# Optimization experiments

Hardware: AMD Instinct MI355X
Metric: run time of the kernel (lower is better)

The kernel has to match this reference:

```python
import jax, jax.numpy as jnp
import numpy as np

VOCAB = 32000
WDIM = 768      # bert-base hidden size, per self.w_dim
H = 512         # lstm_hidden
NUM_CAT = 5
START = 3       # l2ind['SOS']
END = 4         # l2ind['EOS']
T = 2048
NEG = -10000.0


def _lstm_dir(x, Wih, Whh, bih, bhh, reverse):
    # x: [T, WDIM]; torch LSTM gate order: i, f, g, o
    z_in = x @ Wih.T + bih + bhh  # [T, 4H] precompute input projection
    def step(carry, zt):
        h, c = carry
        z = zt + h @ Whh.T
        i, f, g, o = jnp.split(z, 4)
        c = jax.nn.sigmoid(f) * c + jax.nn.sigmoid(i) * jnp.tanh(g)
        h = jax.nn.sigmoid(o) * jnp.tanh(c)
        return (h, c), h
    init = (jnp.zeros((H,), x.dtype), jnp.zeros((H,), x.dtype))
    _, hs = jax.lax.scan(step, init, z_in, reverse=reverse)
    return hs  # [T, H], aligned with input order


def setup_inputs():
    key = jax.random.key(0)
    ks = jax.random.split(key, 13)
    s = 0.05
    sent = jax.random.randint(ks[0], (T,), 0, VOCAB)
    emb = jax.random.normal(ks[1], (VOCAB, WDIM), jnp.float32) * 0.02
    Wih_f = jax.random.normal(ks[2], (4 * H, WDIM), jnp.float32) * s
    Whh_f = jax.random.normal(ks[3], (4 * H, H), jnp.float32) * s
    bih_f = jax.random.normal(ks[4], (4 * H,), jnp.float32) * s
    bhh_f = jax.random.normal(ks[5], (4 * H,), jnp.float32) * s
    Wih_b = jax.random.normal(ks[6], (4 * H, WDIM), jnp.float32) * s
    Whh_b = jax.random.normal(ks[7], (4 * H, H), jnp.float32) * s
    bih_b = jax.random.normal(ks[8], (4 * H,), jnp.float32) * s
    bhh_b = jax.random.normal(ks[9], (4 * H,), jnp.float32) * s
    fc_w = jax.random.normal(ks[10], (NUM_CAT, 2 * H), jnp.float32) * s
    fc_b = jax.random.normal(ks[11], (NUM_CAT,), jnp.float32) * s
    transitions = jax.random.normal(ks[12], (NUM_CAT, NUM_CAT), jnp.float32)
    transitions = transitions.at[START, :].set(NEG).at[:, END].set(NEG)
    return {"sent": sent, "emb": emb,
            "Wih_f": Wih_f, "Whh_f": Whh_f, "bih_f": bih_f, "bhh_f": bhh_f,
            "Wih_b": Wih_b, "Whh_b": Whh_b, "bih_b": bih_b, "bhh_b": bhh_b,
            "fc_w": fc_w, "fc_b": fc_b, "transitions": transitions}


def reference(sent, emb, Wih_f, Whh_f, bih_f, bhh_f, Wih_b, Whh_b, bih_b, bhh_b, fc_w, fc_b, transitions):
    # _get_scores: embedding -> BiLSTM -> fc
    x = emb[sent]                                   # [T, WDIM]
    h_f = _lstm_dir(x, Wih_f, Whh_f, bih_f, bhh_f, reverse=False)
    h_b = _lstm_dir(x, Wih_b, Whh_b, bih_b, bhh_b, reverse=True)
    out = jnp.concatenate([h_f, h_b], axis=-1)      # [T, 2H]
    feats = out @ fc_w.T + fc_b                     # [T, NUM_CAT]

    # _viterbi_decode: transitions[i, j] = score of moving from tag j to tag i
    init = feats[0] + transitions[:, START]         # [NUM_CAT]
    def vstep(layer, feat_t):
        # scores[i, j] = feat_t[i] + transitions[i, j] + layer[j]
        scores = feat_t[:, None] + transitions + layer[None, :]
        return jnp.max(scores, axis=1), jnp.argmax(scores, axis=1)
    layer, parents = jax.lax.scan(vstep, init, feats[1:])  # parents: [T-1, NUM_CAT]

    final = layer + transitions[END]
    idx0 = jnp.argmax(final)
    path_score = jnp.max(final)

    # backtrack (parents[0] of the original loop is all-START and gets popped)
    def btrack(idx, p):
        nxt = p[idx]
        return nxt, nxt
    _, idxs = jax.lax.scan(btrack, idx0, parents, reverse=True)  # [T-1]
    path = jnp.concatenate([idxs, idx0[None]])      # [T]
    return path, path_score
```

## Files before the change

kernel.cpp:

```cpp
#include <hip/hip_runtime.h>

#define TT 2048
#define WD 768
#define HH 512
#define G4 2048
#define NC 5
#define SENT 0xFFFFFFFFu

typedef float f4 __attribute__((ext_vector_type(4)));
typedef unsigned int u4 __attribute__((ext_vector_type(4)));

__global__ __launch_bounds__(256) void zin_gemm(
    const int* __restrict__ sent, const float* __restrict__ emb,
    const float* __restrict__ Wih_f, const float* __restrict__ bih_f, const float* __restrict__ bhh_f,
    const float* __restrict__ Wih_b, const float* __restrict__ bih_b, const float* __restrict__ bhh_b,
    float* __restrict__ zin_f, float* __restrict__ zin_b)
{
    const int dirn = blockIdx.z;
    const float* Wih = dirn ? Wih_b : Wih_f;
    const float* bih = dirn ? bih_b : bih_f;
    const float* bhh = dirn ? bhh_b : bhh_f;
    float* zin = dirn ? zin_b : zin_f;

    __shared__ float As[16][128];
    __shared__ float Bs[16][128];

    const int tid = threadIdx.x;
    const int t0 = blockIdx.y * 128;
    const int g0 = blockIdx.x * 128;
    const int tm = tid >> 4, tn = tid & 15;

    float acc[8][8];
#pragma unroll
    for (int a = 0; a < 8; a++)
#pragma unroll
        for (int b = 0; b < 8; b++) acc[a][b] = 0.f;

    for (int kt = 0; kt < 48; ++kt) {
        const int k0 = kt * 16;
#pragma unroll
        for (int u = 0; u < 2; ++u) {
            const int s = tid * 2 + u;
            const int m = s >> 2, kq = s & 3;
            const int rowA = sent[t0 + m];
            float4 av = *(const float4*)(emb + (size_t)rowA * WD + k0 + kq * 4);
            As[kq * 4 + 0][m] = av.x; As[kq * 4 + 1][m] = av.y;
            As[kq * 4 + 2][m] = av.z; As[kq * 4 + 3][m] = av.w;
            float4 bv = *(const float4*)(Wih + (size_t)(g0 + m) * WD + k0 + kq * 4);
            Bs[kq * 4 + 0][m] = bv.x; Bs[kq * 4 + 1][m] = bv.y;
            Bs[kq * 4 + 2][m] = bv.z; Bs[kq * 4 + 3][m] = bv.w;
        }
        __syncthreads();
#pragma unroll
        for (int kk = 0; kk < 16; ++kk) {
            float4 a0 = *(const float4*)&As[kk][tm * 8];
            float4 a1 = *(const float4*)&As[kk][tm * 8 + 4];
            float4 b0 = *(const float4*)&Bs[kk][tn * 8];
            float4 b1 = *(const float4*)&Bs[kk][tn * 8 + 4];
            float av8[8] = {a0.x, a0.y, a0.z, a0.w, a1.x, a1.y, a1.z, a1.w};
            float bv8[8] = {b0.x, b0.y, b0.z, b0.w, b1.x, b1.y, b1.z, b1.w};
#pragma unroll
            for (int a = 0; a < 8; a++)
#pragma unroll
                for (int b = 0; b < 8; b++) acc[a][b] += av8[a] * bv8[b];
        }
        __syncthreads();
    }
    float bias[8];
#pragma unroll
    for (int b = 0; b < 8; b++) { int g = g0 + tn * 8 + b; bias[b] = bih[g] + bhh[g]; }
#pragma unroll
    for (int a = 0; a < 8; a++) {
        const int t = t0 + tm * 8 + a;
        float* op = zin + (size_t)t * G4 + g0 + tn * 8;
        float4 o0 = {acc[a][0] + bias[0], acc[a][1] + bias[1], acc[a][2] + bias[2], acc[a][3] + bias[3]};
        float4 o1 = {acc[a][4] + bias[4], acc[a][5] + bias[5], acc[a][6] + bias[6], acc[a][7] + bias[7]};
        *(float4*)op = o0; *(float4*)(op + 4) = o1;
    }
}

__global__ __launch_bounds__(256, 1) void lstm_rec(
    const float* __restrict__ zin_f, const float* __restrict__ zin_b,
    const float* __restrict__ Whh_f, const float* __restrict__ Whh_b,
    unsigned int* __restrict__ hw_f, unsigned int* __restrict__ hw_b)
{
    const int bid = blockIdx.x;
    const int d = bid >> 5;
    const int k = bid & 31;
    const float* zin = d ? zin_b : zin_f;
    const float* Whh = d ? Whh_b : Whh_f;
    unsigned int* hw = d ? hw_b : hw_f;

    const int tid = threadIdx.x;
    const int q = tid >> 6;
    const int r = tid & 63;
    const int gate = r >> 4, jj = r & 15;
    const int grow = gate * HH + k * 16 + jj;

    const f4* wp = (const f4*)(Whh + (size_t)grow * HH + q * 128);
    f4 w[32];
#pragma unroll
    for (int i = 0; i < 32; ++i) w[i] = wp[i];
#pragma unroll
    for (int i = 0; i < 32; ++i)
        asm volatile("" : "+a"(w[i]));

    __shared__ float hs[HH];
    __shared__ float zb[256];

    float c = 0.f;
    const int l = tid;
    const int g = l >> 4, j = l & 15;
    const int n16 = k * 16 + j;

    for (int it = 0; it < TT; ++it) {
        const int t = d ? (TT - 1 - it) : it;

        float z = 0.f;
        if (tid < 64) z = zin[(size_t)t * G4 + g * HH + n16];

        if (it > 0 && tid < 64) {
            const int tp = d ? (t + 1) : (t - 1);
            const unsigned int* pa = hw + (size_t)tp * HH + l * 8;
            u4 a0, a1;
            for (;;) {
                asm volatile(
                    "global_load_dwordx4 %0, %2, off sc0 sc1\n\t"
                    "global_load_dwordx4 %1, %2, off offset:16 sc0 sc1\n\t"
                    "s_waitcnt vmcnt(0)"
                    : "=v"(a0), "=v"(a1) : "v"(pa) : "memory");
                if (a0.x != SENT && a0.y != SENT && a0.z != SENT && a0.w != SENT &&
                    a1.x != SENT && a1.y != SENT && a1.z != SENT && a1.w != SENT) break;
            }
            u4* hd = (u4*)(hs + l * 8);
            hd[0] = a0; hd[1] = a1;
        }
        __syncthreads();

#pragma unroll
        for (int i = 0; i < 32; ++i) asm volatile("" : "+a"(w[i]));

        float part = 0.f;
        if (it > 0) {
            const f4* hv = ((const f4*)hs) + (q << 5);
#pragma unroll
            for (int i = 0; i < 32; ++i) {
                f4 h4 = hv[i];
                part += w[i].x * h4.x + w[i].y * h4.y + w[i].z * h4.z + w[i].w * h4.w;
            }
        }
        zb[tid] = part;
        __syncthreads();

        if (tid < 64) {
            float s = zb[l] + zb[64 + l] + zb[128 + l] + zb[192 + l];
            const float pre = z + s;
            float act;
            if (g == 2) act = tanhf(pre);
            else        act = 1.f / (1.f + expf(-pre));
            const float gi = __shfl(act, j);
            const float gf = __shfl(act, j + 16);
            const float gg = __shfl(act, j + 32);
            const float go = __shfl(act, j + 48);
            if (l < 16) {
                c = gf * c + gi * gg;
                const float hval = go * tanhf(c);
                __hip_atomic_store(&hw[(size_t)t * HH + k * 16 + l],
                                   __float_as_uint(hval),
                                   __ATOMIC_RELAXED, __HIP_MEMORY_SCOPE_AGENT);
            }
        }
    }
}

__global__ void feats_kernel(const float* __restrict__ h_f, const float* __restrict__ h_b,
                             const float* __restrict__ fc_w, const float* __restrict__ fc_b,
                             float* __restrict__ feats)
{
    const int t = blockIdx.x;
    const int l = threadIdx.x;
    float acc[NC] = {0.f, 0.f, 0.f, 0.f, 0.f};
    for (int m = 0; m < 16; ++m) {
        const int cg = l + m * 64;
        const float hv = (cg < HH) ? h_f[(size_t)t * HH + cg]
                                   : h_b[(size_t)t * HH + cg - HH];
#pragma unroll
        for (int i = 0; i < NC; i++) acc[i] += hv * fc_w[i * (2 * HH) + cg];
    }
#pragma unroll
    for (int i = 0; i < NC; i++) {
#pragma unroll
        for (int off = 32; off; off >>= 1) acc[i] += __shfl_xor(acc[i], off);
    }
    if (l == 0) {
#pragma unroll
        for (int i = 0; i < NC; i++) feats[(size_t)t * NC + i] = acc[i] + fc_b[i];
    }
}

__global__ void viterbi_kernel(const float* __restrict__ feats,
                               const float* __restrict__ trans,
                               float* __restrict__ out)
{
    __shared__ float fs[TT * NC];
    __shared__ int par[TT];
    __shared__ float pathv[TT];
    const int tid = threadIdx.x;
    for (int i = tid; i < TT * NC; i += 64) fs[i] = feats[i];
    float tr[25];
#pragma unroll
    for (int i = 0; i < 25; i++) tr[i] = trans[i];
    __syncthreads();

    float layer[NC];
#pragma unroll
    for (int i = 0; i < NC; i++) layer[i] = fs[i] + tr[i * 5 + 3];

    for (int s = 0; s < TT - 1; ++s) {
        const float* ft = &fs[(s + 1) * NC];
        float nl[NC]; int pk = 0;
#pragma unroll
        for (int i = 0; i < NC; i++) {
            float best = tr[i * 5 + 0] + layer[0]; int bj = 0;
#pragma unroll
            for (int jj = 1; jj < NC; jj++) {
                const float v = tr[i * 5 + jj] + layer[jj];
                if (v > best) { best = v; bj = jj; }
            }
            nl[i] = ft[i] + best;
            pk |= bj << (3 * i);
        }
#pragma unroll
        for (int i = 0; i < NC; i++) layer[i] = nl[i];
        if (tid == 0) par[s] = pk;
    }
    float best = layer[0] + tr[20]; int idx0 = 0;
#pragma unroll
    for (int jj = 1; jj < NC; jj++) {
        const float v = layer[jj] + tr[20 + jj];
        if (v > best) { best = v; idx0 = jj; }
    }
    __syncthreads();
    if (tid == 0) {
        pathv[TT - 1] = (float)idx0;
        int idx = idx0;
        for (int s = TT - 2; s >= 0; --s) {
            idx = (par[s] >> (3 * idx)) & 7;
            pathv[s] = (float)idx;
        }
        out[TT] = best;
    }
    __syncthreads();
    for (int i = tid; i < TT; i += 64) out[i] = pathv[i];
}

extern "C" void kernel_launch(void* const* d_in, const int* in_sizes, int n_in,
                              void* d_out, int out_size, void* d_ws, size_t ws_size,
                              hipStream_t stream) {
    const int*   sent   = (const int*)d_in[0];
    const float* emb    = (const float*)d_in[1];
    const float* Wih_f  = (const float*)d_in[2];
    const float* Whh_f  = (const float*)d_in[3];
    const float* bih_f  = (const float*)d_in[4];
    const float* bhh_f  = (const float*)d_in[5];
    const float* Wih_b  = (const float*)d_in[6];
    const float* Whh_b  = (const float*)d_in[7];
    const float* bih_b  = (const float*)d_in[8];
    const float* bhh_b  = (const float*)d_in[9];
    const float* fc_w   = (const float*)d_in[10];
    const float* fc_b   = (const float*)d_in[11];
    const float* trans  = (const float*)d_in[12];
    float* out = (float*)d_out;

    char* ws = (char*)d_ws;
    float* zin_f = (float*)ws;
    float* zin_b = (float*)(ws + (size_t)16777216);
    unsigned int* hw_f = (unsigned int*)(ws + (size_t)33554432);
    unsigned int* hw_b = (unsigned int*)(ws + (size_t)37748736);
    float* feats = (float*)(ws + (size_t)41943040);

    hipMemsetAsync(hw_f, 0xFF, (size_t)8388608, stream);

    dim3 gg(G4 / 128, TT / 128, 2);
    zin_gemm<<<gg, 256, 0, stream>>>(sent, emb, Wih_f, bih_f, bhh_f,
                                     Wih_b, bih_b, bhh_b, zin_f, zin_b);

    lstm_rec<<<64, 256, 0, stream>>>(zin_f, zin_b, Whh_f, Whh_b, hw_f, hw_b);

    feats_kernel<<<TT, 64, 0, stream>>>((const float*)hw_f, (const float*)hw_b,
                                        fc_w, fc_b, feats);

    viterbi_kernel<<<1, 64, 0, stream>>>(feats, trans, out);
}
```

Measured before the change: 4.771 ms.

## Co-locate LSTM recurrence blocks per XCD and use L2-scoped polling

The kernel now launches 512 blocks. Each block reads its hardware XCC id and claims a slot. The first two groups of 32 blocks that land on the same XCD become the forward and backward recurrence workers, and the remaining blocks exit. Per-step h exchange then uses sc0-only loads and stores, which stay coherent within the XCD's L2, instead of system-scope sc0 sc1 accesses; after 24 failed spins it falls back to the old fully coherent polling. This is meant to cut the cross-XCD latency on every one of the 2048 serial steps. It relies on dynamic block placement and L2 coherence semantics, and adds a small startup handshake.

```diff
diff --git a/kernel.cpp b/kernel.cpp
--- a/kernel.cpp
+++ b/kernel.cpp
@@ -82,11 +82,39 @@
 __global__ __launch_bounds__(256, 1) void lstm_rec(
     const float* __restrict__ zin_f, const float* __restrict__ zin_b,
     const float* __restrict__ Whh_f, const float* __restrict__ Whh_b,
-    unsigned int* __restrict__ hw_f, unsigned int* __restrict__ hw_b)
+    unsigned int* __restrict__ hw_f, unsigned int* __restrict__ hw_b,
+    unsigned int* __restrict__ ctl)
 {
-    const int bid = blockIdx.x;
-    const int d = bid >> 5;
-    const int k = bid & 31;
+    __shared__ int s_role;
+    if (threadIdx.x == 0) {
+        unsigned int xcc;
+        asm volatile("s_getreg_b32 %0, hwreg(20, 0, 32)" : "=s"(xcc));
+        xcc &= 7u;
+        const unsigned int slot = atomicAdd(&ctl[xcc], 1u) + 1u;
+        const unsigned int grp = slot >> 5, lig = slot & 31u;
+        const unsigned int mytag = (xcc << 8) | grp;
+        if (lig == 31u) {
+            const unsigned int dcl = atomicAdd(&ctl[8], 1u) + 1u;
+            if (dcl < 2u)
+                __hip_atomic_store(&ctl[9 + dcl], mytag,
+                                   __ATOMIC_RELAXED, __HIP_MEMORY_SCOPE_AGENT);
+        }
+        unsigned int c0, c1;
+        do {
+            c0 = __hip_atomic_load(&ctl[9],  __ATOMIC_RELAXED, __HIP_MEMORY_SCOPE_AGENT);
+            c1 = __hip_atomic_load(&ctl[10], __ATOMIC_RELAXED, __HIP_MEMORY_SCOPE_AGENT);
+        } while (c0 == 0xFFFFFFFFu || c1 == 0xFFFFFFFFu);
+        int role = -1;
+        if      (c0 == mytag) role = (int)lig;
+        else if (c1 == mytag) role = 32 + (int)lig;
+        s_role = role;
+    }
+    __syncthreads();
+    const int role = s_role;
+    if (role < 0) return;
+
+    const int d = role >> 5;
+    const int k = role & 31;
     const float* zin = d ? zin_b : zin_f;
     const float* Whh = d ? Whh_b : Whh_f;
     unsigned int* hw = d ? hw_b : hw_f;
@@ -113,6 +141,9 @@
     const int g = l >> 4, j = l & 15;
     const int n16 = k * 16 + j;
 
+#define POLL_OK (a0.x != SENT && a0.y != SENT && a0.z != SENT && a0.w != SENT && \
+                 a1.x != SENT && a1.y != SENT && a1.z != SENT && a1.w != SENT)
+
     for (int it = 0; it < TT; ++it) {
         const int t = d ? (TT - 1 - it) : it;
 
@@ -123,14 +154,25 @@
             const int tp = d ? (t + 1) : (t - 1);
             const unsigned int* pa = hw + (size_t)tp * HH + l * 8;
             u4 a0, a1;
+            int spins = 0;
             for (;;) {
                 asm volatile(
-                    "global_load_dwordx4 %0, %2, off sc0 sc1\n\t"
-                    "global_load_dwordx4 %1, %2, off offset:16 sc0 sc1\n\t"
+                    "global_load_dwordx4 %0, %2, off sc0\n\t"
+                    "global_load_dwordx4 %1, %2, off offset:16 sc0\n\t"
                     "s_waitcnt vmcnt(0)"
                     : "=v"(a0), "=v"(a1) : "v"(pa) : "memory");
-                if (a0.x != SENT && a0.y != SENT && a0.z != SENT && a0.w != SENT &&
-                    a1.x != SENT && a1.y != SENT && a1.z != SENT && a1.w != SENT) break;
+                if (POLL_OK) break;
+                if (++spins > 24) {
+                    for (;;) {
+                        asm volatile(
+                            "global_load_dwordx4 %0, %2, off sc0 sc1\n\t"
+                            "global_load_dwordx4 %1, %2, off offset:16 sc0 sc1\n\t"
+                            "s_waitcnt vmcnt(0)"
+                            : "=v"(a0), "=v"(a1) : "v"(pa) : "memory");
+                        if (POLL_OK) break;
+                    }
+                    break;
+                }
             }
             u4* hd = (u4*)(hs + l * 8);
             hd[0] = a0; hd[1] = a1;
@@ -165,12 +207,14 @@
             if (l < 16) {
                 c = gf * c + gi * gg;
                 const float hval = go * tanhf(c);
-                __hip_atomic_store(&hw[(size_t)t * HH + k * 16 + l],
-                                   __float_as_uint(hval),
-                                   __ATOMIC_RELAXED, __HIP_MEMORY_SCOPE_AGENT);
+                unsigned int hvbits = __float_as_uint(hval);
+                unsigned int* hp = &hw[(size_t)t * HH + k * 16 + l];
+                asm volatile("global_store_dword %0, %1, off sc0"
+                             :: "v"(hp), "v"(hvbits) : "memory");
             }
         }
     }
+#undef POLL_OK
 }
 
 __global__ void feats_kernel(const float* __restrict__ h_f, const float* __restrict__ h_b,
@@ -278,14 +322,16 @@
     unsigned int* hw_f = (unsigned int*)(ws + (size_t)33554432);
     unsigned int* hw_b = (unsigned int*)(ws + (size_t)37748736);
     float* feats = (float*)(ws + (size_t)41943040);
+    unsigned int* ctl = (unsigned int*)(ws + (size_t)41984000);
 
     hipMemsetAsync(hw_f, 0xFF, (size_t)8388608, stream);
+    hipMemsetAsync(ctl, 0xFF, (size_t)128, stream);
 
     dim3 gg(G4 / 128, TT / 128, 2);
     zin_gemm<<<gg, 256, 0, stream>>>(sent, emb, Wih_f, bih_f, bhh_f,
                                      Wih_b, bih_b, bhh_b, zin_f, zin_b);
 
-    lstm_rec<<<64, 256, 0, stream>>>(zin_f, zin_b, Whh_f, Whh_b, hw_f, hw_b);
+    lstm_rec<<<512, 256, 0, stream>>>(zin_f, zin_b, Whh_f, Whh_b, hw_f, hw_b, ctl);
 
     feats_kernel<<<TT, 64, 0, stream>>>((const float*)hw_f, (const float*)hw_b,
                                         fc_w, fc_b, feats);
```

Result: slower. 10.92 ms (+128.9%).

## Spread h polling across all waves, pad h layout, double-buffer reduction scratch

Applied to the files above, without the earlier changes.

All 256 threads now poll the previous timestep's hidden state with 8-byte loads and write it straight into shared memory, instead of one wave polling with 32-byte loads. Two probe loads are kept in flight and checked with a wave-wide vote. The h buffer is padded so each block's 16 outputs sit in a 32-float slot, and the feats kernel indexing is changed to match. The partial-sum scratch is double-buffered so one of the two __syncthreads per step can be removed. This targets the latency of the per-step cross-block handoff, at the cost of more polling traffic and twice the h workspace and memset.

```diff
diff --git a/kernel.cpp b/kernel.cpp
--- a/kernel.cpp
+++ b/kernel.cpp
@@ -9,6 +9,7 @@
 
 typedef float f4 __attribute__((ext_vector_type(4)));
 typedef unsigned int u4 __attribute__((ext_vector_type(4)));
+typedef unsigned int u2 __attribute__((ext_vector_type(2)));
 
 __global__ __launch_bounds__(256) void zin_gemm(
     const int* __restrict__ sent, const float* __restrict__ emb,
@@ -106,36 +107,45 @@
         asm volatile("" : "+a"(w[i]));
 
     __shared__ float hs[HH];
-    __shared__ float zb[256];
+    __shared__ float zb[2][256];
 
     float c = 0.f;
     const int l = tid;
     const int g = l >> 4, j = l & 15;
     const int n16 = k * 16 + j;
 
+    const int pprod = 8 * q + (r >> 3);
+    const int pland = (r & 7) * 2;
+    float2* const hslot = (float2*)hs + (q * 64 + (r >> 3) * 8 + (r & 7));
+
+#define PROBE(dst) \
+    asm volatile("global_load_dwordx2 %0, %1, off sc0 sc1" \
+                 : "+v"(dst) : "v"(pp) : "memory")
+#define WAITV1() asm volatile("s_waitcnt vmcnt(1)" ::: "memory")
+#define WAITV0() asm volatile("s_waitcnt vmcnt(0)" ::: "memory")
+
     for (int it = 0; it < TT; ++it) {
         const int t = d ? (TT - 1 - it) : it;
 
         float z = 0.f;
         if (tid < 64) z = zin[(size_t)t * G4 + g * HH + n16];
 
-        if (it > 0 && tid < 64) {
+        if (it > 0) {
             const int tp = d ? (t + 1) : (t - 1);
-            const unsigned int* pa = hw + (size_t)tp * HH + l * 8;
-            u4 a0, a1;
+            const unsigned int* pp = hw + (size_t)tp * 1024 + pprod * 32 + pland;
+            u2 va = {SENT, SENT}, vb = {SENT, SENT};
+            u2 hv2;
+            PROBE(va);
             for (;;) {
-                asm volatile(
-                    "global_load_dwordx4 %0, %2, off sc0 sc1\n\t"
-                    "global_load_dwordx4 %1, %2, off offset:16 sc0 sc1\n\t"
-                    "s_waitcnt vmcnt(0)"
-                    : "=v"(a0), "=v"(a1) : "v"(pa) : "memory");
-                if (a0.x != SENT && a0.y != SENT && a0.z != SENT && a0.w != SENT &&
-                    a1.x != SENT && a1.y != SENT && a1.z != SENT && a1.w != SENT) break;
+                PROBE(vb);
+                WAITV1();
+                if (__all(va.x != SENT && va.y != SENT)) { hv2 = va; WAITV0(); break; }
+                PROBE(va);
+                WAITV1();
+                if (__all(vb.x != SENT && vb.y != SENT)) { hv2 = vb; WAITV0(); break; }
             }
-            u4* hd = (u4*)(hs + l * 8);
-            hd[0] = a0; hd[1] = a1;
-        }
-        __syncthreads();
+            *hslot = (float2){__uint_as_float(hv2.x), __uint_as_float(hv2.y)};
+        }
 
 #pragma unroll
         for (int i = 0; i < 32; ++i) asm volatile("" : "+a"(w[i]));
@@ -149,11 +159,12 @@
                 part += w[i].x * h4.x + w[i].y * h4.y + w[i].z * h4.z + w[i].w * h4.w;
             }
         }
-        zb[tid] = part;
+        zb[it & 1][tid] = part;
         __syncthreads();
 
         if (tid < 64) {
-            float s = zb[l] + zb[64 + l] + zb[128 + l] + zb[192 + l];
+            const float* zbc = zb[it & 1];
+            float s = zbc[l] + zbc[64 + l] + zbc[128 + l] + zbc[192 + l];
             const float pre = z + s;
             float act;
             if (g == 2) act = tanhf(pre);
@@ -165,12 +176,15 @@
             if (l < 16) {
                 c = gf * c + gi * gg;
                 const float hval = go * tanhf(c);
-                __hip_atomic_store(&hw[(size_t)t * HH + k * 16 + l],
+                __hip_atomic_store(&hw[(size_t)t * 1024 + k * 32 + l],
                                    __float_as_uint(hval),
                                    __ATOMIC_RELAXED, __HIP_MEMORY_SCOPE_AGENT);
             }
         }
     }
+#undef PROBE
+#undef WAITV1
+#undef WAITV0
 }
 
 __global__ void feats_kernel(const float* __restrict__ h_f, const float* __restrict__ h_b,
@@ -182,8 +196,9 @@
     float acc[NC] = {0.f, 0.f, 0.f, 0.f, 0.f};
     for (int m = 0; m < 16; ++m) {
         const int cg = l + m * 64;
-        const float hv = (cg < HH) ? h_f[(size_t)t * HH + cg]
-                                   : h_b[(size_t)t * HH + cg - HH];
+        const int cu = (cg < HH) ? cg : cg - HH;
+        const size_t off = (size_t)t * 1024 + (cu >> 4) * 32 + (cu & 15);
+        const float hv = (cg < HH) ? h_f[off] : h_b[off];
 #pragma unroll
         for (int i = 0; i < NC; i++) acc[i] += hv * fc_w[i * (2 * HH) + cg];
     }
@@ -275,11 +290,11 @@
     char* ws = (char*)d_ws;
     float* zin_f = (float*)ws;
     float* zin_b = (float*)(ws + (size_t)16777216);
-    unsigned int* hw_f = (unsigned int*)(ws + (size_t)33554432);
-    unsigned int* hw_b = (unsigned int*)(ws + (size_t)37748736);
-    float* feats = (float*)(ws + (size_t)41943040);
-
-    hipMemsetAsync(hw_f, 0xFF, (size_t)8388608, stream);
+    unsigned int* hw_f  = (unsigned int*)(ws + (size_t)33554432);
+    unsigned int* hw_b  = (unsigned int*)(ws + (size_t)41943040);
+    float* feats = (float*)(ws + (size_t)50331648);
+
+    hipMemsetAsync(hw_f, 0xFF, (size_t)16777216, stream);
 
     dim3 gg(G4 / 128, TT / 128, 2);
     zin_gemm<<<gg, 256, 0, stream>>>(sent, emb, Wih_f, bih_f, bhh_f,
```

Result: slower. 5.222 ms (+9.4%).

## Use per-block mailbox ring buffers for LSTM hidden-state exchange

Applied to the files above, without the earlier changes.

Each recurrent block now receives the previous hidden state through a private 64-slot ring-buffer mailbox. Producers broadcast each h value into every consumer's mailbox, and consumers reset the slot to the sentinel after reading it. All four waves poll 16-byte chunks in parallel, which removes the first __syncthreads per step; the zb buffer is double-buffered to keep that safe. The cost is eight times more global stores per step, and correctness now depends on ring reuse ordering and on the reset stores becoming visible before the slot is reused.

```diff
diff --git a/kernel.cpp b/kernel.cpp
--- a/kernel.cpp
+++ b/kernel.cpp
@@ -82,7 +82,8 @@
 __global__ __launch_bounds__(256, 1) void lstm_rec(
     const float* __restrict__ zin_f, const float* __restrict__ zin_b,
     const float* __restrict__ Whh_f, const float* __restrict__ Whh_b,
-    unsigned int* __restrict__ hw_f, unsigned int* __restrict__ hw_b)
+    unsigned int* __restrict__ hw_f, unsigned int* __restrict__ hw_b,
+    unsigned int* __restrict__ mb_f, unsigned int* __restrict__ mb_b)
 {
     const int bid = blockIdx.x;
     const int d = bid >> 5;
@@ -90,6 +91,7 @@
     const float* zin = d ? zin_b : zin_f;
     const float* Whh = d ? Whh_b : Whh_f;
     unsigned int* hw = d ? hw_b : hw_f;
+    unsigned int* mb = d ? mb_b : mb_f;
 
     const int tid = threadIdx.x;
     const int q = tid >> 6;
@@ -105,37 +107,38 @@
     for (int i = 0; i < 32; ++i)
         asm volatile("" : "+a"(w[i]));
 
-    __shared__ float hs[HH];
-    __shared__ float zb[256];
+    __shared__ __align__(16) float hs[HH];
+    __shared__ float zb[2][256];
 
     float c = 0.f;
     const int l = tid;
     const int g = l >> 4, j = l & 15;
     const int n16 = k * 16 + j;
 
+    unsigned int* const mbc = mb + (size_t)k * 64 * 512 + q * 128 + r * 4;
+
     for (int it = 0; it < TT; ++it) {
         const int t = d ? (TT - 1 - it) : it;
 
         float z = 0.f;
         if (tid < 64) z = zin[(size_t)t * G4 + g * HH + n16];
 
-        if (it > 0 && tid < 64) {
+        if (it > 0 && r < 32) {
             const int tp = d ? (t + 1) : (t - 1);
-            const unsigned int* pa = hw + (size_t)tp * HH + l * 8;
-            u4 a0, a1;
+            const int sl = tp & 63;
+            const unsigned int* pp = mbc + (size_t)sl * 512;
+            u4 v;
             for (;;) {
-                asm volatile(
-                    "global_load_dwordx4 %0, %2, off sc0 sc1\n\t"
-                    "global_load_dwordx4 %1, %2, off offset:16 sc0 sc1\n\t"
-                    "s_waitcnt vmcnt(0)"
-                    : "=v"(a0), "=v"(a1) : "v"(pa) : "memory");
-                if (a0.x != SENT && a0.y != SENT && a0.z != SENT && a0.w != SENT &&
-                    a1.x != SENT && a1.y != SENT && a1.z != SENT && a1.w != SENT) break;
-            }
-            u4* hd = (u4*)(hs + l * 8);
-            hd[0] = a0; hd[1] = a1;
-        }
-        __syncthreads();
+                asm volatile("global_load_dwordx4 %0, %1, off sc0 sc1\n\t"
+                             "s_waitcnt vmcnt(0)"
+                             : "=v"(v) : "v"(pp) : "memory");
+                if (v.x != SENT && v.y != SENT && v.z != SENT && v.w != SENT) break;
+            }
+            const u4 sv = {SENT, SENT, SENT, SENT};
+            asm volatile("global_store_dwordx4 %0, %1, off sc1"
+                         :: "v"(pp), "v"(sv) : "memory");
+            ((u4*)hs)[q * 32 + r] = v;
+        }
 
 #pragma unroll
         for (int i = 0; i < 32; ++i) asm volatile("" : "+a"(w[i]));
@@ -149,11 +152,12 @@
                 part += w[i].x * h4.x + w[i].y * h4.y + w[i].z * h4.z + w[i].w * h4.w;
             }
         }
-        zb[tid] = part;
+        zb[it & 1][tid] = part;
         __syncthreads();
 
         if (tid < 64) {
-            float s = zb[l] + zb[64 + l] + zb[128 + l] + zb[192 + l];
+            const float* zbc = zb[it & 1];
+            float s = zbc[l] + zbc[64 + l] + zbc[128 + l] + zbc[192 + l];
             const float pre = z + s;
             float act;
             if (g == 2) act = tanhf(pre);
@@ -162,11 +166,22 @@
             const float gf = __shfl(act, j + 16);
             const float gg = __shfl(act, j + 32);
             const float go = __shfl(act, j + 48);
+            float hval = 0.f;
             if (l < 16) {
                 c = gf * c + gi * gg;
-                const float hval = go * tanhf(c);
+                hval = go * tanhf(c);
                 __hip_atomic_store(&hw[(size_t)t * HH + k * 16 + l],
                                    __float_as_uint(hval),
+                                   __ATOMIC_RELAXED, __HIP_MEMORY_SCOPE_AGENT);
+            }
+            const float hb = __shfl(hval, l & 15);
+            const unsigned int hbits = __float_as_uint(hb);
+            const int s2 = t & 63;
+            unsigned int* mp = mb + (size_t)((l >> 4) * 64 + s2) * 512
+                                  + k * 16 + (l & 15);
+#pragma unroll
+            for (int jj2 = 0; jj2 < 8; ++jj2) {
+                __hip_atomic_store(mp + (size_t)jj2 * 4 * 64 * 512, hbits,
                                    __ATOMIC_RELAXED, __HIP_MEMORY_SCOPE_AGENT);
             }
         }
@@ -277,15 +292,18 @@
     float* zin_b = (float*)(ws + (size_t)16777216);
     unsigned int* hw_f = (unsigned int*)(ws + (size_t)33554432);
     unsigned int* hw_b = (unsigned int*)(ws + (size_t)37748736);
-    float* feats = (float*)(ws + (size_t)41943040);
-
-    hipMemsetAsync(hw_f, 0xFF, (size_t)8388608, stream);
+    unsigned int* mb_f = (unsigned int*)(ws + (size_t)41943040);
+    unsigned int* mb_b = (unsigned int*)(ws + (size_t)46137344);
+    float* feats = (float*)(ws + (size_t)50331648);
+
+    hipMemsetAsync(mb_f, 0xFF, (size_t)8388608, stream);
 
     dim3 gg(G4 / 128, TT / 128, 2);
     zin_gemm<<<gg, 256, 0, stream>>>(sent, emb, Wih_f, bih_f, bhh_f,
                                      Wih_b, bih_b, bhh_b, zin_f, zin_b);
 
-    lstm_rec<<<64, 256, 0, stream>>>(zin_f, zin_b, Whh_f, Whh_b, hw_f, hw_b);
+    lstm_rec<<<64, 256, 0, stream>>>(zin_f, zin_b, Whh_f, Whh_b,
+                                     hw_f, hw_b, mb_f, mb_b);
 
     feats_kernel<<<TT, 64, 0, stream>>>((const float*)hw_f, (const float*)hw_b,
                                         fc_w, fc_b, feats);
```

Result: slower. 5.314 ms (+11.4%).
